# Kernel tuning notes

Hardware: AMD Instinct MI355X
Metric: run time of the kernel (lower is better)

## Reference

```python
import jax, jax.numpy as jnp
import numpy as np

NUM_NODES = 100000
NUM_EDGES = 50000
NUM_CONN = 800000
IN_DIM = 256
HIDDEN = 128
EDGE_ATTR_DIM = 17
LN_EPS = 1e-5


def setup_inputs() -> dict:
    key = jax.random.key(0)
    k1, k2, k3, kw1, kb1, kg, kbeta, kw2, kb2 = jax.random.split(key, 9)
    node_features = jax.random.normal(k1, (NUM_NODES, IN_DIM), dtype=jnp.float32)
    nodes = jax.random.randint(k2, (NUM_CONN,), 0, NUM_NODES, dtype=jnp.int64)
    edges = jax.random.randint(k3, (NUM_CONN,), 0, NUM_EDGES, dtype=jnp.int64)
    hyperedge_index = jnp.stack([nodes, edges], axis=0)
    # MLP params (Linear(in,hid) -> LayerNorm -> ReLU -> Dropout(eval:identity) -> Linear(hid,out))
    W1 = jax.random.normal(kw1, (IN_DIM, HIDDEN), dtype=jnp.float32) * (1.0 / np.sqrt(IN_DIM))
    b1 = jax.random.normal(kb1, (HIDDEN,), dtype=jnp.float32) * 0.01
    ln_g = jnp.ones((HIDDEN,), dtype=jnp.float32)
    ln_b = jnp.zeros((HIDDEN,), dtype=jnp.float32)
    W2 = jax.random.normal(kw2, (HIDDEN, EDGE_ATTR_DIM), dtype=jnp.float32) * (1.0 / np.sqrt(HIDDEN))
    b2 = jax.random.normal(kb2, (EDGE_ATTR_DIM,), dtype=jnp.float32) * 0.01
    return {"node_features": node_features, "hyperedge_index": hyperedge_index,
            "W1": W1, "b1": b1, "ln_g": ln_g, "ln_b": ln_b, "W2": W2, "b2": b2}


def reference(node_features, hyperedge_index, W1, b1, ln_g, ln_b, W2, b2):
    nodes = hyperedge_index[0]
    edges = hyperedge_index[1]
    # indices are in-range by construction (torch valid_mask is all-True here)
    gathered = node_features[nodes]                         # [num_conn, in_dim]
    summed = jax.ops.segment_sum(gathered, edges, num_segments=NUM_EDGES)
    counts = jax.ops.segment_sum(jnp.ones(edges.shape, node_features.dtype), edges,
                                 num_segments=NUM_EDGES)
    edge_features = summed / jnp.clip(counts, 1.0)[:, None]  # mean aggregation
    # decoder MLP (dropout inactive in eval)
    h = edge_features @ W1 + b1
    mu = jnp.mean(h, axis=-1, keepdims=True)
    var = jnp.mean(jnp.square(h - mu), axis=-1, keepdims=True)
    h = (h - mu) * jax.lax.rsqrt(var + LN_EPS) * ln_g + ln_b
    h = jax.nn.relu(h)
    return h @ W2 + b2                                      # [num_edges, edge_attr_dim]
```

## Files before the change

### kernel.cpp

```cpp
#include <hip/hip_runtime.h>
#include <hip/hip_bf16.h>
#include <stdint.h>

#define NUM_NODES 100000
#define NUM_EDGES 50000
#define NUM_CONN  800000
#define IN_DIM    256
#define HIDDEN    128
#define EDGE_DIM  17
#define PAD       64

typedef __bf16 bf16x8 __attribute__((ext_vector_type(8)));
typedef float  f32x4  __attribute__((ext_vector_type(4)));


__global__ void prep_kernel(const float* __restrict__ W1, const float* __restrict__ W2,
                            __bf16* __restrict__ w1f, __bf16* __restrict__ w2f,
                            int* __restrict__ counts) {
    int i = blockIdx.x * 256 + threadIdx.x;
    if (i < NUM_EDGES) counts[i] = 0;
    if (i < 4096) {
        int lane = i & 63, t = (i >> 6) & 7, kc2 = i >> 9;
        int m = lane & 15, q = lane >> 4;
        int n = t * 16 + m;
        int kbase = kc2 * 32 + q * 8;
        __bf16* dst = w1f + (size_t)i * 8;
        #pragma unroll
        for (int ki = 0; ki < 8; ++ki)
            dst[ki] = (__bf16)W1[(size_t)(kbase + ki) * HIDDEN + n];
    } else if (i < 4608) {
        int f = i - 4096;
        int lane = f & 63, t = (f >> 6) & 1, ks = f >> 7;
        int m = lane & 15, q = lane >> 4;
        int n = t * 16 + m;
        int kbase = ks * 32 + q * 8;
        __bf16* dst = w2f + (size_t)f * 8;
        #pragma unroll
        for (int ki = 0; ki < 8; ++ki)
            dst[ki] = (n < EDGE_DIM) ? (__bf16)W2[(size_t)(kbase + ki) * EDGE_DIM + n]
                                     : (__bf16)0.0f;
    }
}

__global__ void bucket_kernel(const int* __restrict__ idx,
                              int* __restrict__ counts, int* __restrict__ slots) {
    int i = blockIdx.x * 256 + threadIdx.x;
    if (i >= NUM_CONN / 2) return;
    int4 vn = ((const int4*)idx)[i];
    int4 ve = ((const int4*)(idx + 2 * NUM_CONN))[i];
    int p0 = atomicAdd(&counts[ve.x], 1);
    if (p0 < PAD) slots[(size_t)ve.x * PAD + p0] = vn.x;
    int p1 = atomicAdd(&counts[ve.z], 1);
    if (p1 < PAD) slots[(size_t)ve.z * PAD + p1] = vn.z;
}

__global__ void bucket_kernel_i32(const int* __restrict__ idx,
                                  int* __restrict__ counts, int* __restrict__ slots) {
    int i = blockIdx.x * 256 + threadIdx.x;
    if (i >= NUM_CONN) return;
    int node = idx[i];
    int edge = idx[NUM_CONN + i];
    int pos = atomicAdd(&counts[edge], 1);
    if (pos < PAD) slots[(size_t)edge * PAD + pos] = node;
}

__global__ __launch_bounds__(256, 2) void proj_kernel(const float* __restrict__ nf,
                                                      const __bf16* __restrict__ w1f,
                                                      __bf16* __restrict__ pbf) {
    __shared__ __align__(16) __bf16 lds[32768];
    {
        const uint4* s = (const uint4*)w1f;
        uint4* d = (uint4*)lds;
        #pragma unroll 4
        for (int i = threadIdx.x; i < 4096; i += 256) d[i] = s[i];
    }
    __syncthreads();

    const int wave = threadIdx.x >> 6;
    const int lane = threadIdx.x & 63;
    const int m = lane & 15, q = lane >> 4;
    const int rowbase = blockIdx.x * 256 + wave * 64;
    const bf16x8* frag = (const bf16x8*)lds;

    f32x4 acc[4][8];
    #pragma unroll
    for (int mt = 0; mt < 4; ++mt)
        #pragma unroll
        for (int t = 0; t < 8; ++t) acc[mt][t] = (f32x4){0.f, 0.f, 0.f, 0.f};

    const float* ap[4];
    #pragma unroll
    for (int mt = 0; mt < 4; ++mt) {
        int r = rowbase + mt * 16 + m;
        if (r >= NUM_NODES) r = NUM_NODES - 1;
        ap[mt] = nf + (size_t)r * IN_DIM + q * 8;
    }

    #pragma unroll
    for (int kc2 = 0; kc2 < 8; ++kc2) {
        bf16x8 b[8];
        #pragma unroll
        for (int t = 0; t < 8; ++t) b[t] = frag[(kc2 * 8 + t) * 64 + lane];
        #pragma unroll
        for (int mt = 0; mt < 4; ++mt) {
            float4 f0 = *(const float4*)(ap[mt] + kc2 * 32);
            float4 f1 = *(const float4*)(ap[mt] + kc2 * 32 + 4);
            bf16x8 a;
            a[0] = (__bf16)f0.x; a[1] = (__bf16)f0.y;
            a[2] = (__bf16)f0.z; a[3] = (__bf16)f0.w;
            a[4] = (__bf16)f1.x; a[5] = (__bf16)f1.y;
            a[6] = (__bf16)f1.z; a[7] = (__bf16)f1.w;
            #pragma unroll
            for (int t = 0; t < 8; ++t)
                acc[mt][t] = __builtin_amdgcn_mfma_f32_16x16x32_bf16(a, b[t], acc[mt][t], 0, 0, 0);
        }
    }

    #pragma unroll
    for (int mt = 0; mt < 4; ++mt) {
        int ob = rowbase + mt * 16 + q * 4;
        #pragma unroll
        for (int t = 0; t < 8; ++t)
            #pragma unroll
            for (int r = 0; r < 4; ++r) {
                int orow = ob + r;
                if (orow < NUM_NODES)
                    pbf[(size_t)orow * HIDDEN + t * 16 + m] = (__bf16)acc[mt][t][r];
            }
    }
}

__global__ __launch_bounds__(256) void edge_kernel(const uint4* __restrict__ p4,
        const int* __restrict__ counts, const int* __restrict__ slots,
        const float* __restrict__ b1, const float* __restrict__ ln_g,
        const float* __restrict__ ln_b, uint4* __restrict__ rws) {
    const int wave = threadIdx.x >> 6;
    const int lane = threadIdx.x & 63;
    const int e = blockIdx.x * 4 + wave;
    const int g = lane & 15, rsel = lane >> 4;

    const int c = counts[e];
    const int cc = c < PAD ? c : PAD;
    const float inv = 1.0f / (float)(c > 0 ? c : 1);
    const int slv = slots[(size_t)e * PAD + lane];

    float acc[8];
    #pragma unroll
    for (int d = 0; d < 8; ++d) acc[d] = 0.f;

    for (int j0 = 0; j0 < cc; j0 += 16) {
        uint4 u[4];
        unsigned okm[4];
        #pragma unroll
        for (int qq = 0; qq < 4; ++qq) {
            int j = j0 + 4 * qq + rsel;
            int nd = __shfl(slv, j, 64);
            nd = ((unsigned)nd < NUM_NODES) ? nd : 0;
            u[qq] = p4[(size_t)nd * 16 + g];
            okm[qq] = (j < cc) ? 0xffffffffu : 0u;
        }
        #pragma unroll
        for (int qq = 0; qq < 4; ++qq) {
            uint4 v = u[qq];
            v.x &= okm[qq]; v.y &= okm[qq]; v.z &= okm[qq]; v.w &= okm[qq];
            acc[0] += __uint_as_float(v.x << 16);
            acc[1] += __uint_as_float(v.x & 0xffff0000u);
            acc[2] += __uint_as_float(v.y << 16);
            acc[3] += __uint_as_float(v.y & 0xffff0000u);
            acc[4] += __uint_as_float(v.z << 16);
            acc[5] += __uint_as_float(v.z & 0xffff0000u);
            acc[6] += __uint_as_float(v.w << 16);
            acc[7] += __uint_as_float(v.w & 0xffff0000u);
        }
    }
    #pragma unroll
    for (int d = 0; d < 8; ++d) {
        acc[d] += __shfl_xor(acc[d], 16, 64);
        acc[d] += __shfl_xor(acc[d], 32, 64);
    }

    float4 bA = ((const float4*)b1)[2 * g];
    float4 bB = ((const float4*)b1)[2 * g + 1];
    float h[8];
    h[0] = acc[0] * inv + bA.x; h[1] = acc[1] * inv + bA.y;
    h[2] = acc[2] * inv + bA.z; h[3] = acc[3] * inv + bA.w;
    h[4] = acc[4] * inv + bB.x; h[5] = acc[5] * inv + bB.y;
    h[6] = acc[6] * inv + bB.z; h[7] = acc[7] * inv + bB.w;

    float s = 0.f;
    #pragma unroll
    for (int d = 0; d < 8; ++d) s += h[d];
    #pragma unroll
    for (int off = 8; off > 0; off >>= 1) s += __shfl_xor(s, off, 64);
    float mu = s * (1.0f / 128.0f);

    float dv[8], vv = 0.f;
    #pragma unroll
    for (int d = 0; d < 8; ++d) { dv[d] = h[d] - mu; vv += dv[d] * dv[d]; }
    #pragma unroll
    for (int off = 8; off > 0; off >>= 1) vv += __shfl_xor(vv, off, 64);
    float rs = rsqrtf(vv * (1.0f / 128.0f) + 1e-5f);

    float4 gA = ((const float4*)ln_g)[2 * g];
    float4 gB = ((const float4*)ln_g)[2 * g + 1];
    float4 eA = ((const float4*)ln_b)[2 * g];
    float4 eB = ((const float4*)ln_b)[2 * g + 1];
    float gg[8] = {gA.x, gA.y, gA.z, gA.w, gB.x, gB.y, gB.z, gB.w};
    float ee[8] = {eA.x, eA.y, eA.z, eA.w, eB.x, eB.y, eB.z, eB.w};
    if (rsel == 0) {
        union { __bf16 b[8]; uint4 u; } pk;
        #pragma unroll
        for (int d = 0; d < 8; ++d) {
            float r = dv[d] * rs * gg[d] + ee[d];
            pk.b[d] = (__bf16)(r > 0.f ? r : 0.f);
        }
        rws[(size_t)e * 16 + g] = pk.u;
    }
}

__global__ __launch_bounds__(256) void out_kernel(const __bf16* __restrict__ rws,
        const __bf16* __restrict__ w2f, const float* __restrict__ b2,
        float* __restrict__ out) {
    __shared__ __align__(16) __bf16 lds[4096];
    {
        const uint4* s = (const uint4*)w2f;
        uint4* d = (uint4*)lds;
        #pragma unroll
        for (int i = threadIdx.x; i < 512; i += 256) d[i] = s[i];
    }
    __syncthreads();
    const int wave = threadIdx.x >> 6;
    const int lane = threadIdx.x & 63;
    const int tile = blockIdx.x * 4 + wave;
    if (tile >= NUM_EDGES / 16) return;
    const int m = lane & 15, q = lane >> 4;
    const bf16x8* frag = (const bf16x8*)lds;
    const __bf16* arow = rws + ((size_t)tile * 16 + m) * HIDDEN + q * 8;

    f32x4 acc0 = (f32x4){0.f, 0.f, 0.f, 0.f};
    f32x4 acc1 = (f32x4){0.f, 0.f, 0.f, 0.f};
    #pragma unroll
    for (int s = 0; s < 4; ++s) {
        bf16x8 a = *(const bf16x8*)(arow + s * 32);
        acc0 = __builtin_amdgcn_mfma_f32_16x16x32_bf16(a, frag[(s * 2 + 0) * 64 + lane], acc0, 0, 0, 0);
        acc1 = __builtin_amdgcn_mfma_f32_16x16x32_bf16(a, frag[(s * 2 + 1) * 64 + lane], acc1, 0, 0, 0);
    }
    int rowb = tile * 16 + q * 4;
    float bm = b2[m];
    #pragma unroll
    for (int r = 0; r < 4; ++r) {
        out[(size_t)(rowb + r) * EDGE_DIM + m] = acc0[r] + bm;
        if (m == 0) out[(size_t)(rowb + r) * EDGE_DIM + 16] = acc1[r] + b2[16];
    }
}

extern "C" void kernel_launch(void* const* d_in, const int* in_sizes, int n_in,
                              void* d_out, int out_size, void* d_ws, size_t ws_size,
                              hipStream_t stream) {
    const float* nf  = (const float*)d_in[0];
    const int*   idx = (const int*)d_in[1];
    const float* W1  = (const float*)d_in[2];
    const float* b1  = (const float*)d_in[3];
    const float* g   = (const float*)d_in[4];
    const float* be  = (const float*)d_in[5];
    const float* W2  = (const float*)d_in[6];
    const float* b2  = (const float*)d_in[7];
    float* out = (float*)d_out;

    char* ws = (char*)d_ws;
    __bf16* P      = (__bf16*)ws;
    int*    counts = (int*)(ws + 25600000);
    int*    slots  = (int*)(ws + 25800000);
    __bf16* W1F    = (__bf16*)(ws + 38600000);
    __bf16* W2F    = (__bf16*)(ws + 38665536);
    __bf16* R      = (__bf16*)(ws + 38673728);

    int stride = (in_sizes[1] == 2 * NUM_CONN) ? 1 : 2;

    prep_kernel<<<196, 256, 0, stream>>>(W1, W2, W1F, W2F, counts);
    if (stride == 2)
        bucket_kernel<<<(NUM_CONN / 2 + 255) / 256, 256, 0, stream>>>(idx, counts, slots);
    else
        bucket_kernel_i32<<<(NUM_CONN + 255) / 256, 256, 0, stream>>>(idx, counts, slots);
    proj_kernel<<<(NUM_NODES + 255) / 256, 256, 0, stream>>>(nf, W1F, P);
    edge_kernel<<<NUM_EDGES / 4, 256, 0, stream>>>((const uint4*)P, counts, slots,
                                                   b1, g, be, (uint4*)R);
    out_kernel<<<(NUM_EDGES / 16 + 3) / 4, 256, 0, stream>>>(R, W2F, b2, out);
}
```

Measured before the change: 273.8 us.

## Map one edge per 16-lane group and read W1 fragments from global

The edge aggregation kernel now gives each 16-lane group its own hyperedge, so a wave processes four edges instead of one. This removes the cross-group shuffle reduction, and full 16-neighbour chunks take a fast path with no masking. Each group also loads slot indices per chunk instead of once per wave. The projection kernel drops its LDS staging of W1, reads fragments straight from global memory through the cache, and halves the rows per wave so the launch uses more, smaller blocks. The risks are lane divergence when neighbouring edges have different degrees, and W1 fragment loads now going through the cache instead of LDS.

Measured after the change: 275.6 us. No clear change (+0.7%).

```diff
diff --git a/kernel.cpp b/kernel.cpp
--- a/kernel.cpp
+++ b/kernel.cpp
@@ -64,33 +64,24 @@
     if (pos < PAD) slots[(size_t)edge * PAD + pos] = node;
 }
 
-__global__ __launch_bounds__(256, 2) void proj_kernel(const float* __restrict__ nf,
-                                                      const __bf16* __restrict__ w1f,
-                                                      __bf16* __restrict__ pbf) {
-    __shared__ __align__(16) __bf16 lds[32768];
-    {
-        const uint4* s = (const uint4*)w1f;
-        uint4* d = (uint4*)lds;
-        #pragma unroll 4
-        for (int i = threadIdx.x; i < 4096; i += 256) d[i] = s[i];
-    }
-    __syncthreads();
-
+__global__ __launch_bounds__(256) void proj_kernel(const float* __restrict__ nf,
+                                                   const __bf16* __restrict__ w1f,
+                                                   __bf16* __restrict__ pbf) {
     const int wave = threadIdx.x >> 6;
     const int lane = threadIdx.x & 63;
     const int m = lane & 15, q = lane >> 4;
-    const int rowbase = blockIdx.x * 256 + wave * 64;
-    const bf16x8* frag = (const bf16x8*)lds;
-
-    f32x4 acc[4][8];
-    #pragma unroll
-    for (int mt = 0; mt < 4; ++mt)
+    const int rowbase = blockIdx.x * 128 + wave * 32;
+    const bf16x8* __restrict__ frag = (const bf16x8*)w1f;
+
+    f32x4 acc[2][8];
+    #pragma unroll
+    for (int mt = 0; mt < 2; ++mt)
         #pragma unroll
         for (int t = 0; t < 8; ++t) acc[mt][t] = (f32x4){0.f, 0.f, 0.f, 0.f};
 
-    const float* ap[4];
-    #pragma unroll
-    for (int mt = 0; mt < 4; ++mt) {
+    const float* ap[2];
+    #pragma unroll
+    for (int mt = 0; mt < 2; ++mt) {
         int r = rowbase + mt * 16 + m;
         if (r >= NUM_NODES) r = NUM_NODES - 1;
         ap[mt] = nf + (size_t)r * IN_DIM + q * 8;
@@ -102,7 +93,7 @@
         #pragma unroll
         for (int t = 0; t < 8; ++t) b[t] = frag[(kc2 * 8 + t) * 64 + lane];
         #pragma unroll
-        for (int mt = 0; mt < 4; ++mt) {
+        for (int mt = 0; mt < 2; ++mt) {
             float4 f0 = *(const float4*)(ap[mt] + kc2 * 32);
             float4 f1 = *(const float4*)(ap[mt] + kc2 * 32 + 4);
             bf16x8 a;
@@ -117,7 +108,7 @@
     }
 
     #pragma unroll
-    for (int mt = 0; mt < 4; ++mt) {
+    for (int mt = 0; mt < 2; ++mt) {
         int ob = rowbase + mt * 16 + q * 4;
         #pragma unroll
         for (int t = 0; t < 8; ++t)
@@ -136,47 +127,67 @@
         const float* __restrict__ ln_b, uint4* __restrict__ rws) {
     const int wave = threadIdx.x >> 6;
     const int lane = threadIdx.x & 63;
-    const int e = blockIdx.x * 4 + wave;
-    const int g = lane & 15, rsel = lane >> 4;
+    const int g = lane & 15, ge = lane >> 4;
+    const int e = blockIdx.x * 16 + wave * 4 + ge;
 
     const int c = counts[e];
     const int cc = c < PAD ? c : PAD;
     const float inv = 1.0f / (float)(c > 0 ? c : 1);
-    const int slv = slots[(size_t)e * PAD + lane];
 
     float acc[8];
     #pragma unroll
     for (int d = 0; d < 8; ++d) acc[d] = 0.f;
 
-    for (int j0 = 0; j0 < cc; j0 += 16) {
-        uint4 u[4];
-        unsigned okm[4];
-        #pragma unroll
-        for (int qq = 0; qq < 4; ++qq) {
-            int j = j0 + 4 * qq + rsel;
-            int nd = __shfl(slv, j, 64);
-            nd = ((unsigned)nd < NUM_NODES) ? nd : 0;
-            u[qq] = p4[(size_t)nd * 16 + g];
-            okm[qq] = (j < cc) ? 0xffffffffu : 0u;
+    for (int c0 = 0; c0 < cc; c0 += 16) {
+        int slv = slots[(size_t)e * PAD + c0 + g];
+        int lim = cc - c0; if (lim > 16) lim = 16;
+        if (lim == 16) {
+            #pragma unroll
+            for (int k0 = 0; k0 < 16; k0 += 4) {
+                uint4 u[4];
+                #pragma unroll
+                for (int k = 0; k < 4; ++k) {
+                    int nd = __shfl(slv, ge * 16 + k0 + k, 64);
+                    u[k] = p4[(size_t)nd * 16 + g];
+                }
+                #pragma unroll
+                for (int k = 0; k < 4; ++k) {
+                    acc[0] += __uint_as_float(u[k].x << 16);
+                    acc[1] += __uint_as_float(u[k].x & 0xffff0000u);
+                    acc[2] += __uint_as_float(u[k].y << 16);
+                    acc[3] += __uint_as_float(u[k].y & 0xffff0000u);
+                    acc[4] += __uint_as_float(u[k].z << 16);
+                    acc[5] += __uint_as_float(u[k].z & 0xffff0000u);
+                    acc[6] += __uint_as_float(u[k].w << 16);
+                    acc[7] += __uint_as_float(u[k].w & 0xffff0000u);
+                }
+            }
+        } else {
+            for (int k0 = 0; k0 < lim; k0 += 4) {
+                uint4 u[4];
+                unsigned okm[4];
+                #pragma unroll
+                for (int k = 0; k < 4; ++k) {
+                    int nd = __shfl(slv, ge * 16 + k0 + k, 64);
+                    nd = ((unsigned)nd < NUM_NODES) ? nd : 0;
+                    u[k] = p4[(size_t)nd * 16 + g];
+                    okm[k] = (k0 + k < lim) ? 0xffffffffu : 0u;
+                }
+                #pragma unroll
+                for (int k = 0; k < 4; ++k) {
+                    uint4 v = u[k];
+                    v.x &= okm[k]; v.y &= okm[k]; v.z &= okm[k]; v.w &= okm[k];
+                    acc[0] += __uint_as_float(v.x << 16);
+                    acc[1] += __uint_as_float(v.x & 0xffff0000u);
+                    acc[2] += __uint_as_float(v.y << 16);
+                    acc[3] += __uint_as_float(v.y & 0xffff0000u);
+                    acc[4] += __uint_as_float(v.z << 16);
+                    acc[5] += __uint_as_float(v.z & 0xffff0000u);
+                    acc[6] += __uint_as_float(v.w << 16);
+                    acc[7] += __uint_as_float(v.w & 0xffff0000u);
+                }
+            }
         }
-        #pragma unroll
-        for (int qq = 0; qq < 4; ++qq) {
-            uint4 v = u[qq];
-            v.x &= okm[qq]; v.y &= okm[qq]; v.z &= okm[qq]; v.w &= okm[qq];
-            acc[0] += __uint_as_float(v.x << 16);
-            acc[1] += __uint_as_float(v.x & 0xffff0000u);
-            acc[2] += __uint_as_float(v.y << 16);
-            acc[3] += __uint_as_float(v.y & 0xffff0000u);
-            acc[4] += __uint_as_float(v.z << 16);
-            acc[5] += __uint_as_float(v.z & 0xffff0000u);
-            acc[6] += __uint_as_float(v.w << 16);
-            acc[7] += __uint_as_float(v.w & 0xffff0000u);
-        }
-    }
-    #pragma unroll
-    for (int d = 0; d < 8; ++d) {
-        acc[d] += __shfl_xor(acc[d], 16, 64);
-        acc[d] += __shfl_xor(acc[d], 32, 64);
     }
 
     float4 bA = ((const float4*)b1)[2 * g];
@@ -207,15 +218,13 @@
     float4 eB = ((const float4*)ln_b)[2 * g + 1];
     float gg[8] = {gA.x, gA.y, gA.z, gA.w, gB.x, gB.y, gB.z, gB.w};
     float ee[8] = {eA.x, eA.y, eA.z, eA.w, eB.x, eB.y, eB.z, eB.w};
-    if (rsel == 0) {
-        union { __bf16 b[8]; uint4 u; } pk;
-        #pragma unroll
-        for (int d = 0; d < 8; ++d) {
-            float r = dv[d] * rs * gg[d] + ee[d];
-            pk.b[d] = (__bf16)(r > 0.f ? r : 0.f);
-        }
-        rws[(size_t)e * 16 + g] = pk.u;
-    }
+    union { __bf16 b[8]; uint4 u; } pk;
+    #pragma unroll
+    for (int d = 0; d < 8; ++d) {
+        float r = dv[d] * rs * gg[d] + ee[d];
+        pk.b[d] = (__bf16)(r > 0.f ? r : 0.f);
+    }
+    rws[(size_t)e * 16 + g] = pk.u;
 }
 
 __global__ __launch_bounds__(256) void out_kernel(const __bf16* __restrict__ rws,
@@ -282,8 +291,8 @@
         bucket_kernel<<<(NUM_CONN / 2 + 255) / 256, 256, 0, stream>>>(idx, counts, slots);
     else
         bucket_kernel_i32<<<(NUM_CONN + 255) / 256, 256, 0, stream>>>(idx, counts, slots);
-    proj_kernel<<<(NUM_NODES + 255) / 256, 256, 0, stream>>>(nf, W1F, P);
-    edge_kernel<<<NUM_EDGES / 4, 256, 0, stream>>>((const uint4*)P, counts, slots,
-                                                   b1, g, be, (uint4*)R);
+    proj_kernel<<<(NUM_NODES + 127) / 128, 256, 0, stream>>>(nf, W1F, P);
+    edge_kernel<<<NUM_EDGES / 16, 256, 0, stream>>>((const uint4*)P, counts, slots,
+                                                    b1, g, be, (uint4*)R);
     out_kernel<<<(NUM_EDGES / 16 + 3) / 4, 256, 0, stream>>>(R, W2F, b2, out);
 }
```
